# Optimization experiments

Hardware: AMD Instinct MI355X
Metric: run time of the kernel (lower is better)

## Reference

```python
import jax, jax.numpy as jnp
import numpy as np

N = 100000       # nodes
E = 1600000      # edges
F_IN = 128       # input features
HID = 64         # hidden dim
CLS = 16         # classes


def setup_inputs() -> dict:
    key = jax.random.key(0)
    k = jax.random.split(key, 6)
    x = jax.random.normal(k[0], (N, F_IN), dtype=jnp.float32)
    src = jax.random.randint(k[1], (E,), 0, N, dtype=jnp.int32)
    dst = jax.random.randint(k[2], (E,), 0, N, dtype=jnp.int32)
    edge_index = jnp.stack([src, dst], axis=0)
    W1 = jax.random.normal(k[3], (F_IN, HID), dtype=jnp.float32) * (1.0 / np.sqrt(F_IN))
    b1 = jnp.zeros((HID,), dtype=jnp.float32)
    W2 = jax.random.normal(k[4], (HID, CLS), dtype=jnp.float32) * (1.0 / np.sqrt(HID))
    b2 = jnp.zeros((CLS,), dtype=jnp.float32)
    return {"x": x, "edge_index": edge_index, "W1": W1, "b1": b1, "W2": W2, "b2": b2}


def gcn_conv(x, W, b, src, dst, n_nodes):
    # GCNConv(normalize=True): h = W x; out_i = sum_{j->i} h_j / sqrt(d_i d_j) + h_i / d_i + b
    # (self-loops added with weight 1; deg includes the self-loop)
    h = x @ W                                             # [N, out]
    ones = jnp.ones(src.shape[0], dtype=x.dtype)
    deg = jax.ops.segment_sum(ones, dst, num_segments=n_nodes) + 1.0   # [N]
    dinv = deg ** -0.5
    norm = dinv[src] * dinv[dst]                          # [E]
    msg = h[src] * norm[:, None]                          # [E, out] gather
    out = jax.ops.segment_sum(msg, dst, num_segments=n_nodes)          # scatter-add
    out = out + h * (1.0 / deg)[:, None] + b              # self-loop term + bias
    return out


def reference(x, edge_index, W1, b1, W2, b2):
    src, dst = edge_index[0], edge_index[1]
    n = x.shape[0]
    h = jax.nn.relu(gcn_conv(x, W1, b1, src, dst, n))
    # dropout(p=0.5) is identity in eval mode
    h = jax.nn.relu(gcn_conv(h, W2, b2, src, dst, n))
    return jax.nn.log_softmax(h, axis=-1)
```

## Files before the change

kernel.cpp:

```cpp
#include <hip/hip_runtime.h>


typedef unsigned short u16;
typedef __attribute__((ext_vector_type(8))) short short8;
typedef __attribute__((ext_vector_type(4))) float f32x4;

#define CAP 4096

__device__ __forceinline__ float bf2f(u16 u) {
  return __uint_as_float(((unsigned int)u) << 16);
}
__device__ __forceinline__ u16 f2bf(float f) {
  unsigned int u = __float_as_uint(f);
  u += 0x7fffu + ((u >> 16) & 1u);
  return (u16)(u >> 16);
}

__global__ __launch_bounds__(256) void kconvw(const void* __restrict__ W1r,
                                              const void* __restrict__ b1r,
                                              const void* __restrict__ W2r,
                                              const void* __restrict__ b2r,
                                              u16* __restrict__ W1b,
                                              float* __restrict__ b1f,
                                              float* __restrict__ W2f,
                                              float* __restrict__ b2f,
                                              int* __restrict__ mode) {
  __shared__ float red[4];
  __shared__ int smode;
  const u16* w = (const u16*)W1r;
  float mx = 0.f;
  for (int i = threadIdx.x; i < 8192; i += 256) {
    float av = fabsf(bf2f(w[i]));
    if (!(av <= 1e6f)) av = 3e38f;
    mx = fmaxf(mx, av);
  }
  #pragma unroll
  for (int off = 32; off >= 1; off >>= 1) mx = fmaxf(mx, __shfl_xor(mx, off, 64));
  if ((threadIdx.x & 63) == 0) red[threadIdx.x >> 6] = mx;
  __syncthreads();
  if (threadIdx.x == 0) {
    float m2 = fmaxf(fmaxf(red[0], red[1]), fmaxf(red[2], red[3]));
    smode = (m2 > 1e6f) ? 1 : 0;
    if (blockIdx.x == 0) mode[0] = smode;
  }
  __syncthreads();
  int m = smode;
  int gid = blockIdx.x * 256 + threadIdx.x, stride = gridDim.x * 256;
  for (int i = gid; i < 8192; i += stride)
    W1b[i] = m ? f2bf(((const float*)W1r)[i]) : ((const u16*)W1r)[i];
  for (int i = gid; i < 1024; i += stride)
    W2f[i] = m ? ((const float*)W2r)[i] : bf2f(((const u16*)W2r)[i]);
  for (int i = gid; i < 64; i += stride)
    b1f[i] = m ? ((const float*)b1r)[i] : bf2f(((const u16*)b1r)[i]);
  for (int i = gid; i < 16; i += stride)
    b2f[i] = m ? ((const float*)b2r)[i] : bf2f(((const u16*)b2r)[i]);
}

__global__ __launch_bounds__(512) void kpart(const int* __restrict__ src,
                                             const int* __restrict__ dst,
                                             int* __restrict__ cursor,
                                             int* __restrict__ etmp,
                                             int E, int NB) {
  __shared__ int hist[1024], basep[1024];
  int tid = threadIdx.x;
  for (int i = tid; i < 1024; i += 512) hist[i] = 0;
  __syncthreads();
  int e0 = blockIdx.x * 8192 + tid * 16;
  int pk[16], off[16], cb[16];
  if (e0 + 15 < E) {
    int4 s4[4], d4[4];
    #pragma unroll
    for (int u = 0; u < 4; ++u) {
      s4[u] = ((const int4*)(src + e0))[u];
      d4[u] = ((const int4*)(dst + e0))[u];
    }
    const int* sp = (const int*)s4;
    const int* dp = (const int*)d4;
    #pragma unroll
    for (int k = 0; k < 16; ++k) {
      int s = sp[k], d = dp[k];
      cb[k] = d >> 7;
      pk[k] = (s << 7) | (d & 127);
      off[k] = atomicAdd(&hist[cb[k]], 1);
    }
  } else {
    #pragma unroll
    for (int k = 0; k < 16; ++k) {
      int e = e0 + k;
      cb[k] = -1;
      if (e < E) {
        int s = src[e], d = dst[e];
        cb[k] = d >> 7;
        pk[k] = (s << 7) | (d & 127);
        off[k] = atomicAdd(&hist[cb[k]], 1);
      }
    }
  }
  __syncthreads();
  for (int i = tid; i < NB; i += 512)
    if (hist[i]) basep[i] = atomicAdd(&cursor[i], hist[i]);
  __syncthreads();
  if (e0 + 15 < E) {
    #pragma unroll
    for (int k = 0; k < 16; ++k)
      etmp[cb[k] * CAP + basep[cb[k]] + off[k]] = pk[k];
  } else {
    #pragma unroll
    for (int k = 0; k < 16; ++k)
      if (cb[k] >= 0) etmp[cb[k] * CAP + basep[cb[k]] + off[k]] = pk[k];
  }
}

__global__ __launch_bounds__(512) void kfine(int* __restrict__ etmp,
                                             const int* __restrict__ cursor,
                                             int2* __restrict__ rowse,
                                             float* __restrict__ dinv, int N) {
  __shared__ int eL[CAP];
  __shared__ int hist[128], curs[128];
  int bk = blockIdx.x, tid = threadIdx.x;
  int cnt = cursor[bk];
  int base = bk * CAP;
  if (tid < 128) hist[tid] = 0;
  __syncthreads();
  for (int i = tid; i < cnt; i += 512) {
    int pk = etmp[base + i];
    eL[i] = pk;
    atomicAdd(&hist[pk & 127], 1);
  }
  __syncthreads();
  if (tid < 64) {
    int v0 = hist[tid], v1 = hist[tid + 64];
    int s0 = v0;
    #pragma unroll
    for (int off = 1; off < 64; off <<= 1) {
      int t = __shfl_up(s0, off, 64);
      if (tid >= off) s0 += t;
    }
    int tot0 = __shfl(s0, 63, 64);
    int s1 = v1;
    #pragma unroll
    for (int off = 1; off < 64; off <<= 1) {
      int t = __shfl_up(s1, off, 64);
      if (tid >= off) s1 += t;
    }
    s1 += tot0;
    int e0x = s0 - v0, e1x = s1 - v1;
    int node0 = (bk << 7) + tid, node1 = node0 + 64;
    if (node0 < N) {
      rowse[node0] = make_int2(base + e0x, base + e0x + v0);
      dinv[node0] = rsqrtf((float)(v0 + 1));
    }
    if (node1 < N) {
      rowse[node1] = make_int2(base + e1x, base + e1x + v1);
      dinv[node1] = rsqrtf((float)(v1 + 1));
    }
    curs[tid] = e0x;
    curs[tid + 64] = e1x;
  }
  __syncthreads();
  for (int i = tid; i < cnt; i += 512) {
    int pk = eL[i];
    int pos = atomicAdd(&curs[pk & 127], 1);
    etmp[base + pos] = pk >> 7;
  }
}

__global__ __launch_bounds__(256) void kgemm1(const void* __restrict__ xraw,
                                              const u16* __restrict__ W1b,
                                              const int* __restrict__ mode,
                                              const float* __restrict__ dinv,
                                              u16* __restrict__ h1s, int n) {
  int mflag = mode[0];
  int wid = blockIdx.x * 4 + (threadIdx.x >> 6);
  int row0 = wid * 16;
  if (row0 >= n) return;
  int lane = threadIdx.x & 63;
  int m = lane & 15, q = lane >> 4;

  short8 bfrag[4][4];
  for (int jb = 0; jb < 4; ++jb)
    for (int kb = 0; kb < 4; ++kb) {
      short8 f;
      #pragma unroll
      for (int j = 0; j < 8; ++j)
        f[j] = (short)W1b[(kb * 32 + q * 8 + j) * 64 + jb * 16 + m];
      bfrag[jb][kb] = f;
    }

  f32x4 acc[4];
  #pragma unroll
  for (int jb = 0; jb < 4; ++jb) acc[jb] = (f32x4){0.f, 0.f, 0.f, 0.f};

  #pragma unroll
  for (int kb = 0; kb < 4; ++kb) {
    short8 a;
    if (mflag) {
      const float* xf = (const float*)xraw + (size_t)(row0 + m) * 128 + kb * 32 + q * 8;
      float4 u0 = ((const float4*)xf)[0];
      float4 u1 = ((const float4*)xf)[1];
      a[0] = (short)f2bf(u0.x); a[1] = (short)f2bf(u0.y);
      a[2] = (short)f2bf(u0.z); a[3] = (short)f2bf(u0.w);
      a[4] = (short)f2bf(u1.x); a[5] = (short)f2bf(u1.y);
      a[6] = (short)f2bf(u1.z); a[7] = (short)f2bf(u1.w);
    } else {
      a = *(const short8*)((const u16*)xraw + (size_t)(row0 + m) * 128 + kb * 32 + q * 8);
    }
    #pragma unroll
    for (int jb = 0; jb < 4; ++jb)
      acc[jb] = __builtin_amdgcn_mfma_f32_16x16x32_bf16(a, bfrag[jb][kb], acc[jb], 0, 0, 0);
  }

  #pragma unroll
  for (int r = 0; r < 4; ++r) {
    float dv = dinv[row0 + q * 4 + r];
    #pragma unroll
    for (int jb = 0; jb < 4; ++jb)
      h1s[(row0 + q * 4 + r) * 64 + jb * 16 + m] = f2bf(acc[jb][r] * dv);
  }
}

__global__ __launch_bounds__(256) void kagg1(
    const u16* __restrict__ h1s, const int* __restrict__ esort,
    const int2* __restrict__ rowse, const float* __restrict__ dinv,
    const float* __restrict__ b1f, const float* __restrict__ W2f,
    u16* __restrict__ h2sb, int n) {
  __shared__ float W2s[64 * 17];
  int tid = threadIdx.x;
  for (int i = tid; i < 1024; i += 256)
    W2s[(i >> 4) * 17 + (i & 15)] = W2f[i];
  __syncthreads();

  int lane = tid & 63, wv = tid >> 6;
  int ql = lane & 15, q = lane >> 4;
  int node = blockIdx.x * 16 + wv * 4 + q;
  if (node >= n) node = n - 1;
  int2 se = rowse[node];
  int beg = se.x, end = se.y;
  const uint2* h1v = (const uint2*)h1s;
  uint2 sg = h1v[node * 16 + ql];
  float a0 = 0.f, a1 = 0.f, a2 = 0.f, a3 = 0.f;

  for (int base = beg; base < end; base += 16) {
    int idx = base + ql;
    int eidx = esort[(idx < end) ? idx : (end - 1)];
    int cnt = min(16, end - base);
    int k = 0;
    for (; k + 8 <= cnt; k += 8) {
      uint2 g[8];
      #pragma unroll
      for (int p = 0; p < 8; ++p) {
        int s = __shfl(eidx, k + p, 16);
        g[p] = h1v[s * 16 + ql];
      }
      #pragma unroll
      for (int p = 0; p < 8; ++p) {
        a0 += bf2f((u16)(g[p].x & 0xffff));
        a1 += bf2f((u16)(g[p].x >> 16));
        a2 += bf2f((u16)(g[p].y & 0xffff));
        a3 += bf2f((u16)(g[p].y >> 16));
      }
    }
    for (; k < cnt; ++k) {
      int s = __shfl(eidx, k, 16);
      uint2 g = h1v[s * 16 + ql];
      a0 += bf2f((u16)(g.x & 0xffff));
      a1 += bf2f((u16)(g.x >> 16));
      a2 += bf2f((u16)(g.y & 0xffff));
      a3 += bf2f((u16)(g.y >> 16));
    }
  }

  float dv = dinv[node];
  float4 b1v = ((const float4*)b1f)[ql];
  float vr0 = fmaxf(dv * (a0 + bf2f((u16)(sg.x & 0xffff))) + b1v.x, 0.f);
  float vr1 = fmaxf(dv * (a1 + bf2f((u16)(sg.x >> 16))) + b1v.y, 0.f);
  float vr2 = fmaxf(dv * (a2 + bf2f((u16)(sg.y & 0xffff))) + b1v.z, 0.f);
  float vr3 = fmaxf(dv * (a3 + bf2f((u16)(sg.y >> 16))) + b1v.w, 0.f);

  float p = 0.f;
  #pragma unroll
  for (int j = 0; j < 64; ++j) {
    float vj;
    switch (j & 3) {
      case 0: vj = __shfl(vr0, j >> 2, 16); break;
      case 1: vj = __shfl(vr1, j >> 2, 16); break;
      case 2: vj = __shfl(vr2, j >> 2, 16); break;
      default: vj = __shfl(vr3, j >> 2, 16); break;
    }
    p = fmaf(vj, W2s[j * 17 + ql], p);
  }
  h2sb[node * 16 + ql] = f2bf(p * dv);
}

__global__ __launch_bounds__(256) void kagg2(
    const u16* __restrict__ h2sb, const int* __restrict__ esort,
    const int2* __restrict__ rowse, const float* __restrict__ dinv,
    const float* __restrict__ b2f, const int* __restrict__ mode,
    void* __restrict__ out, int n) {
  int mflag = mode[0];
  int tid = threadIdx.x;
  int lane = tid & 63, wv = tid >> 6;
  int ol = lane & 7, oc = lane >> 3;
  int node = blockIdx.x * 32 + wv * 8 + oc;
  if (node >= n) node = n - 1;
  int2 se = rowse[node];
  int beg = se.x, end = se.y;
  const unsigned int* h2v = (const unsigned int*)h2sb;
  unsigned int sg = h2v[node * 8 + ol];
  float ax = 0.f, ay = 0.f;

  for (int base = beg; base < end; base += 8) {
    int idx = base + ol;
    int eidx = esort[(idx < end) ? idx : (end - 1)];
    int cnt = min(8, end - base);
    int k = 0;
    for (; k + 8 <= cnt; k += 8) {
      unsigned int g[8];
      #pragma unroll
      for (int p = 0; p < 8; ++p) {
        int s = __shfl(eidx, k + p, 8);
        g[p] = h2v[s * 8 + ol];
      }
      #pragma unroll
      for (int p = 0; p < 8; ++p) {
        ax += bf2f((u16)(g[p] & 0xffff));
        ay += bf2f((u16)(g[p] >> 16));
      }
    }
    for (; k < cnt; ++k) {
      int s = __shfl(eidx, k, 8);
      unsigned int g = h2v[s * 8 + ol];
      ax += bf2f((u16)(g & 0xffff));
      ay += bf2f((u16)(g >> 16));
    }
  }

  float dv = dinv[node];
  float2 b2v = ((const float2*)b2f)[ol];
  float vx = fmaxf(dv * (ax + bf2f((u16)(sg & 0xffff))) + b2v.x, 0.f);
  float vy = fmaxf(dv * (ay + bf2f((u16)(sg >> 16))) + b2v.y, 0.f);

  float m = fmaxf(vx, vy);
  #pragma unroll
  for (int off = 1; off <= 4; off <<= 1) m = fmaxf(m, __shfl_xor(m, off, 8));
  float ex = __expf(vx - m) + __expf(vy - m);
  #pragma unroll
  for (int off = 1; off <= 4; off <<= 1) ex += __shfl_xor(ex, off, 8);
  float lg = __logf(ex);
  float rx = vx - m - lg, ry = vy - m - lg;
  if (mflag) ((float2*)out)[(size_t)node * 8 + ol] = make_float2(rx, ry);
  else ((unsigned int*)out)[(size_t)node * 8 + ol] =
         (unsigned int)f2bf(rx) | ((unsigned int)f2bf(ry) << 16);
}

extern "C" void kernel_launch(void* const* d_in, const int* in_sizes, int n_in,
                              void* d_out, int out_size, void* d_ws, size_t ws_size,
                              hipStream_t stream) {
  const void* x  = d_in[0];
  const int* ei  = (const int*)d_in[1];
  const void* W1 = d_in[2];
  const void* b1 = d_in[3];
  const void* W2 = d_in[4];
  const void* b2 = d_in[5];

  const int N = in_sizes[0] / 128;
  const int E = in_sizes[1] / 2;
  const int* src = ei;
  const int* dst = ei + E;
  const int NB = (N + 127) >> 7;

  char* ws = (char*)d_ws;
  size_t off = 0;
  auto alloc = [&](size_t bytes) -> char* {
    char* p = ws + off;
    off = (off + bytes + 255) & ~(size_t)255;
    return p;
  };
  u16*   h1s    = (u16*)  alloc((size_t)N * 64 * 2);
  u16*   h2sb   = (u16*)  alloc((size_t)N * 16 * 2);
  int*   etmp   = (int*)  alloc((size_t)NB * CAP * 4);
  float* dinv   = (float*)alloc((size_t)N * 4);
  int2*  rowse  = (int2*) alloc((size_t)N * 8);
  int*   cursor = (int*)  alloc((size_t)NB * 4);
  u16*   W1b    = (u16*)  alloc(8192 * 2);
  float* W2f    = (float*)alloc(1024 * 4);
  float* b1f    = (float*)alloc(64 * 4);
  float* b2f    = (float*)alloc(16 * 4);
  int*   mode   = (int*)  alloc(4);

  hipMemsetAsync(cursor, 0, (size_t)NB * 4, stream);

  kconvw<<<32, 256, 0, stream>>>(W1, b1, W2, b2, W1b, b1f, W2f, b2f, mode);

  kpart<<<(E + 8191) / 8192, 512, 0, stream>>>(src, dst, cursor, etmp, E, NB);
  kfine<<<NB, 512, 0, stream>>>(etmp, cursor, rowse, dinv, N);

  int tiles = (N + 15) / 16;
  kgemm1<<<(tiles + 3) / 4, 256, 0, stream>>>(x, W1b, mode, dinv, h1s, N);
  kagg1<<<(N + 15) / 16, 256, 0, stream>>>(h1s, etmp, rowse, dinv, b1f, W2f, h2sb, N);
  kagg2<<<(N + 31) / 32, 256, 0, stream>>>(h2sb, etmp, rowse, dinv, b2f, mode, d_out, N);
}
```

Before: 219.5 us.

## Fuse fine bucket sort into layer-1 aggregation and use MFMA for W2 projection

The fine counting sort moves out of kfine, which now only computes degrees for dinv. The sort now runs inside a new per-bucket aggregation kernel that keeps sorted source indices in shared memory, writes esort and rowse for layer 2, and applies the 64x16 W2 projection with bf16 MFMA instead of a shuffle-and-FMA loop. The float-to-bf16 conversion of x switches to the packed HIP intrinsic. The aim is to drop the separate etmp reread and writeback and the shuffle-heavy projection. The cost is 512-thread blocks holding 32KB of LDS each, one block per 128-node bucket, which may cut occupancy and parallelism in the gather phase, and an extra bf16 rounding of the activations before the projection.

```diff
diff --git a/kernel.cpp b/kernel.cpp
--- a/kernel.cpp
+++ b/kernel.cpp
@@ -1,4 +1,5 @@
 #include <hip/hip_runtime.h>
+#include <hip/hip_bf16.h>
 
 
 typedef unsigned short u16;
@@ -22,7 +23,7 @@
                                               const void* __restrict__ b2r,
                                               u16* __restrict__ W1b,
                                               float* __restrict__ b1f,
-                                              float* __restrict__ W2f,
+                                              u16* __restrict__ W2b,
                                               float* __restrict__ b2f,
                                               int* __restrict__ mode) {
   __shared__ float red[4];
@@ -49,7 +50,7 @@
   for (int i = gid; i < 8192; i += stride)
     W1b[i] = m ? f2bf(((const float*)W1r)[i]) : ((const u16*)W1r)[i];
   for (int i = gid; i < 1024; i += stride)
-    W2f[i] = m ? ((const float*)W2r)[i] : bf2f(((const u16*)W2r)[i]);
+    W2b[i] = m ? f2bf(((const float*)W2r)[i]) : ((const u16*)W2r)[i];
   for (int i = gid; i < 64; i += stride)
     b1f[i] = m ? ((const float*)b1r)[i] : bf2f(((const u16*)b1r)[i]);
   for (int i = gid; i < 16; i += stride)
@@ -111,58 +112,20 @@
   }
 }
 
-__global__ __launch_bounds__(512) void kfine(int* __restrict__ etmp,
+__global__ __launch_bounds__(512) void kfine(const int* __restrict__ etmp,
                                              const int* __restrict__ cursor,
-                                             int2* __restrict__ rowse,
                                              float* __restrict__ dinv, int N) {
-  __shared__ int eL[CAP];
-  __shared__ int hist[128], curs[128];
+  __shared__ int hist[128];
   int bk = blockIdx.x, tid = threadIdx.x;
-  int cnt = cursor[bk];
-  int base = bk * CAP;
+  int cnt = cursor[bk], base = bk * CAP;
   if (tid < 128) hist[tid] = 0;
   __syncthreads();
-  for (int i = tid; i < cnt; i += 512) {
-    int pk = etmp[base + i];
-    eL[i] = pk;
-    atomicAdd(&hist[pk & 127], 1);
-  }
-  __syncthreads();
-  if (tid < 64) {
-    int v0 = hist[tid], v1 = hist[tid + 64];
-    int s0 = v0;
-    #pragma unroll
-    for (int off = 1; off < 64; off <<= 1) {
-      int t = __shfl_up(s0, off, 64);
-      if (tid >= off) s0 += t;
-    }
-    int tot0 = __shfl(s0, 63, 64);
-    int s1 = v1;
-    #pragma unroll
-    for (int off = 1; off < 64; off <<= 1) {
-      int t = __shfl_up(s1, off, 64);
-      if (tid >= off) s1 += t;
-    }
-    s1 += tot0;
-    int e0x = s0 - v0, e1x = s1 - v1;
-    int node0 = (bk << 7) + tid, node1 = node0 + 64;
-    if (node0 < N) {
-      rowse[node0] = make_int2(base + e0x, base + e0x + v0);
-      dinv[node0] = rsqrtf((float)(v0 + 1));
-    }
-    if (node1 < N) {
-      rowse[node1] = make_int2(base + e1x, base + e1x + v1);
-      dinv[node1] = rsqrtf((float)(v1 + 1));
-    }
-    curs[tid] = e0x;
-    curs[tid + 64] = e1x;
-  }
-  __syncthreads();
-  for (int i = tid; i < cnt; i += 512) {
-    int pk = eL[i];
-    int pos = atomicAdd(&curs[pk & 127], 1);
-    etmp[base + pos] = pk >> 7;
-  }
+  for (int i = tid; i < cnt; i += 512)
+    atomicAdd(&hist[etmp[base + i] & 127], 1);
+  __syncthreads();
+  int node = (bk << 7) + tid;
+  if (tid < 128 && node < N)
+    dinv[node] = rsqrtf((float)(hist[tid] + 1));
 }
 
 __global__ __launch_bounds__(256) void kgemm1(const void* __restrict__ xraw,
@@ -198,10 +161,18 @@
       const float* xf = (const float*)xraw + (size_t)(row0 + m) * 128 + kb * 32 + q * 8;
       float4 u0 = ((const float4*)xf)[0];
       float4 u1 = ((const float4*)xf)[1];
-      a[0] = (short)f2bf(u0.x); a[1] = (short)f2bf(u0.y);
-      a[2] = (short)f2bf(u0.z); a[3] = (short)f2bf(u0.w);
-      a[4] = (short)f2bf(u1.x); a[5] = (short)f2bf(u1.y);
-      a[6] = (short)f2bf(u1.z); a[7] = (short)f2bf(u1.w);
+      __hip_bfloat162 p0 = __float22bfloat162_rn(make_float2(u0.x, u0.y));
+      __hip_bfloat162 p1 = __float22bfloat162_rn(make_float2(u0.z, u0.w));
+      __hip_bfloat162 p2 = __float22bfloat162_rn(make_float2(u1.x, u1.y));
+      __hip_bfloat162 p3 = __float22bfloat162_rn(make_float2(u1.z, u1.w));
+      unsigned int w0 = *(const unsigned int*)&p0;
+      unsigned int w1 = *(const unsigned int*)&p1;
+      unsigned int w2 = *(const unsigned int*)&p2;
+      unsigned int w3 = *(const unsigned int*)&p3;
+      a[0] = (short)(w0 & 0xffff); a[1] = (short)(w0 >> 16);
+      a[2] = (short)(w1 & 0xffff); a[3] = (short)(w1 >> 16);
+      a[4] = (short)(w2 & 0xffff); a[5] = (short)(w2 >> 16);
+      a[6] = (short)(w3 & 0xffff); a[7] = (short)(w3 >> 16);
     } else {
       a = *(const short8*)((const u16*)xraw + (size_t)(row0 + m) * 128 + kb * 32 + q * 8);
     }
@@ -219,39 +190,95 @@
   }
 }
 
-__global__ __launch_bounds__(256) void kagg1(
-    const u16* __restrict__ h1s, const int* __restrict__ esort,
-    const int2* __restrict__ rowse, const float* __restrict__ dinv,
-    const float* __restrict__ b1f, const float* __restrict__ W2f,
-    u16* __restrict__ h2sb, int n) {
-  __shared__ float W2s[64 * 17];
+__global__ __launch_bounds__(512) void kagg1f(
+    const u16* __restrict__ h1s, const int* __restrict__ etmp,
+    const int* __restrict__ cursor, const float* __restrict__ dinv,
+    const float* __restrict__ b1f, const u16* __restrict__ W2b,
+    int* __restrict__ esort, int2* __restrict__ rowse,
+    u16* __restrict__ h2sb, int N) {
+  __shared__ int eL[CAP];
+  __shared__ int eS[CAP];
+  __shared__ int hist[128], starts[128], curs[128];
+  __shared__ float sdinv[128];
+
   int tid = threadIdx.x;
-  for (int i = tid; i < 1024; i += 256)
-    W2s[(i >> 4) * 17 + (i & 15)] = W2f[i];
-  __syncthreads();
+  int bk = blockIdx.x;
+  int base = bk * CAP;
+  int cnt = cursor[bk];
+  int node0 = bk << 7;
+
+  if (tid < 128) {
+    hist[tid] = 0;
+    int nd = node0 + tid;
+    sdinv[tid] = (nd < N) ? dinv[nd] : 0.f;
+  }
+  __syncthreads();
+  for (int i = tid; i < cnt; i += 512) {
+    int pk = etmp[base + i];
+    eL[i] = pk;
+    atomicAdd(&hist[pk & 127], 1);
+  }
+  __syncthreads();
+  if (tid < 64) {
+    int v0 = hist[tid], v1 = hist[tid + 64];
+    int s0 = v0;
+    #pragma unroll
+    for (int off = 1; off < 64; off <<= 1) {
+      int t = __shfl_up(s0, off, 64);
+      if (tid >= off) s0 += t;
+    }
+    int tot0 = __shfl(s0, 63, 64);
+    int s1 = v1;
+    #pragma unroll
+    for (int off = 1; off < 64; off <<= 1) {
+      int t = __shfl_up(s1, off, 64);
+      if (tid >= off) s1 += t;
+    }
+    s1 += tot0;
+    int e0x = s0 - v0, e1x = s1 - v1;
+    starts[tid] = e0x;  curs[tid] = e0x;
+    starts[tid + 64] = e1x;  curs[tid + 64] = e1x;
+    int n0 = node0 + tid, n1 = n0 + 64;
+    if (n0 < N) rowse[n0] = make_int2(base + e0x, base + e0x + v0);
+    if (n1 < N) rowse[n1] = make_int2(base + e1x, base + e1x + v1);
+  }
+  __syncthreads();
+  for (int i = tid; i < cnt; i += 512) {
+    int pk = eL[i];
+    int pos = atomicAdd(&curs[pk & 127], 1);
+    int sidx = pk >> 7;
+    eS[pos] = sidx;
+    esort[base + pos] = sidx;
+  }
 
   int lane = tid & 63, wv = tid >> 6;
-  int ql = lane & 15, q = lane >> 4;
-  int node = blockIdx.x * 16 + wv * 4 + q;
-  if (node >= n) node = n - 1;
-  int2 se = rowse[node];
-  int beg = se.x, end = se.y;
+  int m16 = lane & 15, q = lane >> 4;
+  short8 bw0, bw1;
+  #pragma unroll
+  for (int j = 0; j < 8; ++j) {
+    bw0[j] = (short)W2b[(q * 8 + j) * 16 + m16];
+    bw1[j] = (short)W2b[(32 + q * 8 + j) * 16 + m16];
+  }
+  __syncthreads();
+
+  float* rowsL = (float*)eL;
   const uint2* h1v = (const uint2*)h1s;
-  uint2 sg = h1v[node * 16 + ql];
-  float a0 = 0.f, a1 = 0.f, a2 = 0.f, a3 = 0.f;
-
-  for (int base = beg; base < end; base += 16) {
-    int idx = base + ql;
-    int eidx = esort[(idx < end) ? idx : (end - 1)];
-    int cnt = min(16, end - base);
-    int k = 0;
-    for (; k + 8 <= cnt; k += 8) {
+  int ql = m16;
+
+  for (int pass = 0; pass < 4; ++pass) {
+    int nl = pass * 32 + wv * 4 + q;
+    int nd = node0 + nl;
+    int cn = (nd < N) ? nd : node0;
+    int rs = starts[nl], deg = hist[nl];
+    float a0 = 0.f, a1 = 0.f, a2 = 0.f, a3 = 0.f;
+    int k = rs, ke = rs + deg;
+    for (; k + 8 <= ke; k += 8) {
+      int sI[8];
       uint2 g[8];
       #pragma unroll
-      for (int p = 0; p < 8; ++p) {
-        int s = __shfl(eidx, k + p, 16);
-        g[p] = h1v[s * 16 + ql];
-      }
+      for (int p = 0; p < 8; ++p) sI[p] = eS[k + p];
+      #pragma unroll
+      for (int p = 0; p < 8; ++p) g[p] = h1v[sI[p] * 16 + ql];
       #pragma unroll
       for (int p = 0; p < 8; ++p) {
         a0 += bf2f((u16)(g[p].x & 0xffff));
@@ -260,36 +287,47 @@
         a3 += bf2f((u16)(g[p].y >> 16));
       }
     }
-    for (; k < cnt; ++k) {
-      int s = __shfl(eidx, k, 16);
+    for (; k < ke; ++k) {
+      int s = eS[k];
       uint2 g = h1v[s * 16 + ql];
       a0 += bf2f((u16)(g.x & 0xffff));
       a1 += bf2f((u16)(g.x >> 16));
       a2 += bf2f((u16)(g.y & 0xffff));
       a3 += bf2f((u16)(g.y >> 16));
     }
-  }
-
-  float dv = dinv[node];
-  float4 b1v = ((const float4*)b1f)[ql];
-  float vr0 = fmaxf(dv * (a0 + bf2f((u16)(sg.x & 0xffff))) + b1v.x, 0.f);
-  float vr1 = fmaxf(dv * (a1 + bf2f((u16)(sg.x >> 16))) + b1v.y, 0.f);
-  float vr2 = fmaxf(dv * (a2 + bf2f((u16)(sg.y & 0xffff))) + b1v.z, 0.f);
-  float vr3 = fmaxf(dv * (a3 + bf2f((u16)(sg.y >> 16))) + b1v.w, 0.f);
-
-  float p = 0.f;
-  #pragma unroll
-  for (int j = 0; j < 64; ++j) {
-    float vj;
-    switch (j & 3) {
-      case 0: vj = __shfl(vr0, j >> 2, 16); break;
-      case 1: vj = __shfl(vr1, j >> 2, 16); break;
-      case 2: vj = __shfl(vr2, j >> 2, 16); break;
-      default: vj = __shfl(vr3, j >> 2, 16); break;
-    }
-    p = fmaf(vj, W2s[j * 17 + ql], p);
-  }
-  h2sb[node * 16 + ql] = f2bf(p * dv);
+    uint2 sg = h1v[cn * 16 + ql];
+    float dv = sdinv[nl];
+    float4 bv = ((const float4*)b1f)[ql];
+    float4 vr;
+    vr.x = fmaxf(dv * (a0 + bf2f((u16)(sg.x & 0xffff))) + bv.x, 0.f);
+    vr.y = fmaxf(dv * (a1 + bf2f((u16)(sg.x >> 16))) + bv.y, 0.f);
+    vr.z = fmaxf(dv * (a2 + bf2f((u16)(sg.y & 0xffff))) + bv.z, 0.f);
+    vr.w = fmaxf(dv * (a3 + bf2f((u16)(sg.y >> 16))) + bv.w, 0.f);
+
+    *(float4*)&rowsL[(wv * 4 + q) * 68 + 4 * ql] = vr;
+    __builtin_amdgcn_wave_barrier();
+
+    const float* ar = &rowsL[(wv * 4 + (m16 & 3)) * 68];
+    bool rv = (m16 < 4);
+    short8 af0, af1;
+    #pragma unroll
+    for (int j = 0; j < 8; ++j) {
+      af0[j] = rv ? (short)f2bf(ar[q * 8 + j]) : (short)0;
+      af1[j] = rv ? (short)f2bf(ar[32 + q * 8 + j]) : (short)0;
+    }
+    f32x4 c = (f32x4){0.f, 0.f, 0.f, 0.f};
+    c = __builtin_amdgcn_mfma_f32_16x16x32_bf16(af0, bw0, c, 0, 0, 0);
+    c = __builtin_amdgcn_mfma_f32_16x16x32_bf16(af1, bw1, c, 0, 0, 0);
+    if (q == 0) {
+      #pragma unroll
+      for (int r = 0; r < 4; ++r) {
+        int nl2 = pass * 32 + wv * 4 + r;
+        int nd2 = node0 + nl2;
+        if (nd2 < N) h2sb[nd2 * 16 + m16] = f2bf(c[r] * sdinv[nl2]);
+      }
+    }
+    __builtin_amdgcn_wave_barrier();
+  }
 }
 
 __global__ __launch_bounds__(256) void kagg2(
@@ -379,24 +417,27 @@
   u16*   h1s    = (u16*)  alloc((size_t)N * 64 * 2);
   u16*   h2sb   = (u16*)  alloc((size_t)N * 16 * 2);
   int*   etmp   = (int*)  alloc((size_t)NB * CAP * 4);
+  int*   esort  = (int*)  alloc((size_t)NB * CAP * 4);
+  int2*  rowse  = (int2*) alloc((size_t)N * 8);
   float* dinv   = (float*)alloc((size_t)N * 4);
-  int2*  rowse  = (int2*) alloc((size_t)N * 8);
   int*   cursor = (int*)  alloc((size_t)NB * 4);
   u16*   W1b    = (u16*)  alloc(8192 * 2);
-  float* W2f    = (float*)alloc(1024 * 4);
+  u16*   W2b    = (u16*)  alloc(1024 * 2);
   float* b1f    = (float*)alloc(64 * 4);
   float* b2f    = (float*)alloc(16 * 4);
   int*   mode   = (int*)  alloc(4);
 
   hipMemsetAsync(cursor, 0, (size_t)NB * 4, stream);
 
-  kconvw<<<32, 256, 0, stream>>>(W1, b1, W2, b2, W1b, b1f, W2f, b2f, mode);
+  kconvw<<<32, 256, 0, stream>>>(W1, b1, W2, b2, W1b, b1f, W2b, b2f, mode);
 
   kpart<<<(E + 8191) / 8192, 512, 0, stream>>>(src, dst, cursor, etmp, E, NB);
-  kfine<<<NB, 512, 0, stream>>>(etmp, cursor, rowse, dinv, N);
+  kfine<<<NB, 512, 0, stream>>>(etmp, cursor, dinv, N);
 
   int tiles = (N + 15) / 16;
   kgemm1<<<(tiles + 3) / 4, 256, 0, stream>>>(x, W1b, mode, dinv, h1s, N);
-  kagg1<<<(N + 15) / 16, 256, 0, stream>>>(h1s, etmp, rowse, dinv, b1f, W2f, h2sb, N);
-  kagg2<<<(N + 31) / 32, 256, 0, stream>>>(h2sb, etmp, rowse, dinv, b2f, mode, d_out, N);
-}
+  kagg1f<<<NB, 512, 0, stream>>>(h1s, etmp, cursor, dinv, b1f, W2b,
+                                 esort, rowse, h2sb, N);
+  kagg2<<<(N + 31) / 32, 256, 0, stream>>>(h2sb, esort, rowse, dinv, b2f, mode,
+                                           d_out, N);
+}
```

New measurement: 204.9 us. 1.07x faster.
